# Performance work log

Hardware: AMD Instinct MI355X
Metric: run time of the kernel (lower is better)

The kernel has to match this reference:

```python
import jax, jax.numpy as jnp
import numpy as np


def blockdiag_matmul(x, w):
    """Block-diagonal (Monarch) linear: w has shape (nblocks, out_blk, in_blk);
    x has shape (..., nblocks*in_blk); returns (..., nblocks*out_blk)."""
    nb, q, p = w.shape
    lead = x.shape[:-1]
    xb = x.reshape(-1, nb, p)  # (tokens, nblocks, in_blk)
    out = jnp.einsum('bnp,nqp->bnq', xb, w)  # per-block matmul
    return out.reshape(*lead, nb * q)


def setup_inputs() -> dict:
    key = jax.random.key(0)
    k_x, k1, k2, k3 = jax.random.split(key, 4)
    B, S, D = 4, 4096, 2048
    NB, FF = 4, 8192  # nblocks, adjusted intermediate size
    # Kaiming-uniform-like scale for block weights (fan_in = D or FF per block-row)
    s1 = 1.0 / np.sqrt(D)
    s2 = 1.0 / np.sqrt(FF)
    return {
        'x': jax.random.normal(k_x, (B, S, D), dtype=jnp.float32),
        'w1': jax.random.normal(k1, (NB, FF // NB, D // NB), dtype=jnp.float32) * s1,
        'w3': jax.random.normal(k3, (NB, FF // NB, D // NB), dtype=jnp.float32) * s1,
        'w2': jax.random.normal(k2, (NB, D // NB, FF // NB), dtype=jnp.float32) * s2,
    }


def reference(x, w1, w3, w2):
    # SwiGLU MLP: w2(silu(w1(x)) * w3(x)), all projections block-diagonal
    gate = jax.nn.silu(blockdiag_matmul(x, w1))
    up = blockdiag_matmul(x, w3)
    return blockdiag_matmul(gate * up, w2)
```

## Files before the change

### kernel.cpp

```cpp
#include <hip/hip_runtime.h>
#include <cstdint>

typedef __attribute__((ext_vector_type(8))) short bf16x8;
typedef __attribute__((ext_vector_type(4))) float f32x4;
typedef unsigned short u16;

#define RD(p) (*(const bf16x8*)(p))

__device__ inline u16 f2bf(float f) {
  union { float f; unsigned int u; } v; v.f = f;
  unsigned int u = v.u;
  unsigned int r = (u + 0x7fffu + ((u >> 16) & 1u)) >> 16;
  return (u16)r;
}

__device__ inline void gload_lds16(const u16* g, u16* l) {
  __builtin_amdgcn_global_load_lds(
      (const __attribute__((address_space(1))) void*)g,
      (__attribute__((address_space(3))) void*)l, 16, 0, 0);
}

#define PH_BEGIN() \
  __builtin_amdgcn_s_barrier(); \
  asm volatile("s_waitcnt lgkmcnt(0)" ::: "memory"); \
  __builtin_amdgcn_s_setprio(1)
#define PH_END() \
  __builtin_amdgcn_s_setprio(0); \
  __builtin_amdgcn_s_barrier()

__global__ void cvt_f32_bf16(const float* __restrict__ src, u16* __restrict__ dst, int n8) {
  int i = blockIdx.x * blockDim.x + threadIdx.x;
  int stride = gridDim.x * blockDim.x;
  for (; i < n8; i += stride) {
    const float4* s = (const float4*)(src + (size_t)i * 8);
    float4 a = s[0], b = s[1];
    union { u16 h[8]; uint4 v; } o;
    o.h[0] = f2bf(a.x); o.h[1] = f2bf(a.y); o.h[2] = f2bf(a.z); o.h[3] = f2bf(a.w);
    o.h[4] = f2bf(b.x); o.h[5] = f2bf(b.y); o.h[6] = f2bf(b.z); o.h[7] = f2bf(b.w);
    *(uint4*)(dst + (size_t)i * 8) = o.v;
  }
}

__launch_bounds__(512, 2)
__global__ void gemm_gateup8(const u16* __restrict__ xb, const u16* __restrict__ w1b,
                             const u16* __restrict__ w3b, u16* __restrict__ hout) {
  constexpr int NT = 8;
  __shared__ __attribute__((aligned(16))) u16 lA[2][256 * 64];
  __shared__ __attribute__((aligned(16))) u16 lB[2][2][128 * 64];

  int bid = blockIdx.x;
  int sw = (bid & 7) * 512 + (bid >> 3);
  int nblk = sw >> 10;
  int rem = sw & 1023;
  int mt = rem >> 4, nt = rem & 15;

  int tid = threadIdx.x, w = tid >> 6, ln = tid & 63;
  int wr = w >> 1, wc = w & 1;
  int l15 = ln & 15, l4 = ln >> 4;
  int lr = ln >> 3, ln8 = ln & 7;

  int cx0 = ((l4 ^ (l15 & 7)) << 4);
  int cx1 = (((4 + l4) ^ (l15 & 7)) << 4);
  int aOff0 = (wr * 64 + l15) * 128 + cx0;
  int aOff1 = (wr * 64 + l15) * 128 + cx1;
  int bOff0 = (wc * 64 + l15) * 128 + cx0;
  int bOff1 = (wc * 64 + l15) * 128 + cx1;

  int u0t = w * 8, u1t = 64 + w * 8;
  int rbA0 = ((u0t >> 5) << 6) + (u0t & 31);
  int rbA1 = ((u1t >> 5) << 6) + (u1t & 31);
  int dA0 = rbA0 * 128, dA1 = rbA1 * 128;
  int dB0 = u0t * 128, dB1 = u1t * 128;
  int gaA0 = rbA0 * 2048, gaA1 = rbA1 * 2048;
  int gaB0 = u0t * 512, gaB1 = u1t * 512;
  int swzg = (ln8 ^ lr) << 3;

  const u16* gA  = xb  + (size_t)(mt * 256) * 2048 + nblk * 512 + lr * 2048 + swzg;
  const u16* gB1 = w1b + (size_t)nblk * (2048 * 512) + (size_t)(nt * 128) * 512 + lr * 512 + swzg;
  const u16* gB3 = w3b + (size_t)nblk * (2048 * 512) + (size_t)(nt * 128) * 512 + lr * 512 + swzg;

  f32x4 acc1[4][4], acc3[4][4];
#pragma unroll
  for (int i = 0; i < 4; i++)
#pragma unroll
    for (int j = 0; j < 4; j++) {
      acc1[i][j] = (f32x4){0.f, 0.f, 0.f, 0.f};
      acc3[i][j] = (f32x4){0.f, 0.f, 0.f, 0.f};
    }

  gload_lds16(gA + gaA0,          (u16*)((char*)lA + dA0));
  gload_lds16(gA + gaA1,          (u16*)((char*)lA + dA1));
  gload_lds16(gB3 + gaB0,         (u16*)((char*)lB + 16384 + dB0));
  gload_lds16(gB3 + gaB1,         (u16*)((char*)lB + 16384 + dB1));
  gload_lds16(gA + gaA0 + 65536,  (u16*)((char*)lA + dA0 + 4096));
  gload_lds16(gA + gaA1 + 65536,  (u16*)((char*)lA + dA1 + 4096));
  gload_lds16(gB1 + gaB0,         (u16*)((char*)lB + dB0));
  gload_lds16(gB1 + gaB1,         (u16*)((char*)lB + dB1));
  gload_lds16(gA + 64 + gaA0,         (u16*)((char*)lA + 32768 + dA0));
  gload_lds16(gA + 64 + gaA1,         (u16*)((char*)lA + 32768 + dA1));
  gload_lds16(gB3 + 64 + gaB0,        (u16*)((char*)lB + 32768 + 16384 + dB0));
  gload_lds16(gB3 + 64 + gaB1,        (u16*)((char*)lB + 32768 + 16384 + dB1));
  gload_lds16(gA + 64 + gaA0 + 65536, (u16*)((char*)lA + 32768 + dA0 + 4096));
  gload_lds16(gA + 64 + gaA1 + 65536, (u16*)((char*)lA + 32768 + dA1 + 4096));
  gA += 128; gB3 += 128; gB1 += 64;
  asm volatile("s_waitcnt vmcnt(6)" ::: "memory");
  __builtin_amdgcn_s_barrier();

  int sCur = 0, sNxt = 32768;
  bf16x8 aT[2][2], aH[2][2], b1[4][2], b3[4][2];

  for (int kt = 0; kt < NT; ++kt) {
    const char* pA0 = (const char*)lA + (sCur + aOff0);
    const char* pA1 = (const char*)lA + (sCur + aOff1);
    const char* pB0 = (const char*)lB + (sCur + bOff0);
    const char* pB1p = (const char*)lB + (sCur + bOff1);
    bool s1 = (kt + 1 < NT), s2 = (kt + 2 < NT);

#pragma unroll
    for (int f = 0; f < 2; ++f) {
      aT[f][0] = RD(pA0 + f * 2048); aT[f][1] = RD(pA1 + f * 2048);
    }
#pragma unroll
    for (int g = 0; g < 4; ++g) {
      b1[g][0] = RD(pB0 + g * 2048); b1[g][1] = RD(pB1p + g * 2048);
    }
    if (s1) {
      gload_lds16(gB1 + gaB0, (u16*)((char*)lB + sNxt + dB0));
      gload_lds16(gB1 + gaB1, (u16*)((char*)lB + sNxt + dB1));
    }
    asm volatile("s_waitcnt lgkmcnt(8)" ::: "memory");
    PH_BEGIN();
#pragma unroll
    for (int f = 0; f < 2; ++f)
#pragma unroll
      for (int g = 0; g < 4; ++g)
#pragma unroll
        for (int ks = 0; ks < 2; ++ks)
          acc1[f][g] = __builtin_amdgcn_mfma_f32_16x16x32_bf16(aT[f][ks], b1[g][ks], acc1[f][g], 0, 0, 0);
    PH_END();

#pragma unroll
    for (int g = 0; g < 4; ++g) {
      b3[g][0] = RD(pB0 + 16384 + g * 2048); b3[g][1] = RD(pB1p + 16384 + g * 2048);
    }
    if (s2) {
      gload_lds16(gA + gaA0, (u16*)((char*)lA + sCur + dA0));
      gload_lds16(gA + gaA1, (u16*)((char*)lA + sCur + dA1));
    }
    PH_BEGIN();
#pragma unroll
    for (int f = 0; f < 2; ++f)
#pragma unroll
      for (int g = 0; g < 4; ++g)
#pragma unroll
        for (int ks = 0; ks < 2; ++ks)
          acc3[f][g] = __builtin_amdgcn_mfma_f32_16x16x32_bf16(aT[f][ks], b3[g][ks], acc3[f][g], 0, 0, 0);
    PH_END();

#pragma unroll
    for (int f = 0; f < 2; ++f) {
      aH[f][0] = RD(pA0 + 4096 + f * 2048); aH[f][1] = RD(pA1 + 4096 + f * 2048);
    }
    if (s2) {
      gload_lds16(gB3 + gaB0, (u16*)((char*)lB + sCur + 16384 + dB0));
      gload_lds16(gB3 + gaB1, (u16*)((char*)lB + sCur + 16384 + dB1));
    }
    PH_BEGIN();
#pragma unroll
    for (int f = 0; f < 2; ++f)
#pragma unroll
      for (int g = 0; g < 4; ++g)
#pragma unroll
        for (int ks = 0; ks < 2; ++ks)
          acc1[2 + f][g] = __builtin_amdgcn_mfma_f32_16x16x32_bf16(aH[f][ks], b1[g][ks], acc1[2 + f][g], 0, 0, 0);
    PH_END();

    if (s2) {
      gload_lds16(gA + gaA0 + 65536, (u16*)((char*)lA + sCur + dA0 + 4096));
      gload_lds16(gA + gaA1 + 65536, (u16*)((char*)lA + sCur + dA1 + 4096));
    }
    PH_BEGIN();
#pragma unroll
    for (int f = 0; f < 2; ++f)
#pragma unroll
      for (int g = 0; g < 4; ++g)
#pragma unroll
        for (int ks = 0; ks < 2; ++ks)
          acc3[2 + f][g] = __builtin_amdgcn_mfma_f32_16x16x32_bf16(aH[f][ks], b3[g][ks], acc3[2 + f][g], 0, 0, 0);
    __builtin_amdgcn_s_setprio(0);
    if (kt < NT - 2)       asm volatile("s_waitcnt vmcnt(6)" ::: "memory");
    else if (kt == NT - 2) asm volatile("s_waitcnt vmcnt(0)" ::: "memory");
    __builtin_amdgcn_s_barrier();
    gA += 64; gB1 += 64; gB3 += 64;
    sCur ^= 32768; sNxt ^= 32768;
  }

  u16* Hb = hout + (size_t)(mt * 256 + wr * 64) * 8192 + nblk * 2048 + nt * 128 + wc * 64;
#pragma unroll
  for (int f = 0; f < 4; ++f)
#pragma unroll
    for (int g = 0; g < 4; ++g) {
      int col = g * 16 + l15;
#pragma unroll
      for (int r = 0; r < 4; ++r) {
        int row = f * 16 + l4 * 4 + r;
        float gate = acc1[f][g][r];
        float up = acc3[f][g][r];
        float s = gate * __builtin_amdgcn_rcpf(1.f + __expf(-gate));
        Hb[(size_t)row * 8192 + col] = f2bf(s * up);
      }
    }
}

__launch_bounds__(512, 2)
__global__ void gemm_down8(const u16* __restrict__ hmat, const u16* __restrict__ w2b,
                           float* __restrict__ out) {
  constexpr int NT = 32;
  __shared__ __attribute__((aligned(16))) u16 lA[2][256 * 64];
  __shared__ __attribute__((aligned(16))) u16 lB[2][256 * 64];

  int bid = blockIdx.x;
  int sw = (bid & 7) * 64 + (bid >> 3);
  int nblk = sw >> 7;
  int rem = sw & 127;
  int mt = rem >> 1, nt = rem & 1;

  int tid = threadIdx.x, w = tid >> 6, ln = tid & 63;
  int mi = w >> 2, nj = w & 3;
  int l15 = ln & 15, l4 = ln >> 4;
  int lr = ln >> 3, ln8 = ln & 7;

  int cx0 = ((l4 ^ (l15 & 7)) << 4);
  int cx1 = (((4 + l4) ^ (l15 & 7)) << 4);
  int aOff0 = (mi * 128 + l15) * 128 + cx0;
  int aOff1 = (mi * 128 + l15) * 128 + cx1;
  int bOff0 = (nj * 64 + l15) * 128 + cx0;
  int bOff1 = (nj * 64 + l15) * 128 + cx1;

  int u0t = w * 8, u1t = 64 + w * 8;
  int dA0 = u0t * 128, dA1 = (64 + u1t) * 128;
  int rbB0 = ((u0t >> 5) << 6) + (u0t & 31);
  int rbB1 = ((u1t >> 5) << 6) + (u1t & 31);
  int dB0 = rbB0 * 128, dB1 = rbB1 * 128;
  int gaA0 = u0t * 8192, gaA1 = (64 + u1t) * 8192;
  int gaB0 = rbB0 * 2048, gaB1 = rbB1 * 2048;
  int swzg = (ln8 ^ lr) << 3;

  const u16* gA = hmat + (size_t)(mt * 256) * 8192 + nblk * 2048 + lr * 8192 + swzg;
  const u16* gB = w2b + (size_t)nblk * (512 * 2048) + (size_t)(nt * 256) * 2048 + lr * 2048 + swzg;

  f32x4 acc[8][4];
#pragma unroll
  for (int i = 0; i < 8; i++)
#pragma unroll
    for (int j = 0; j < 4; j++) acc[i][j] = (f32x4){0.f, 0.f, 0.f, 0.f};

  gload_lds16(gA + gaA0,           (u16*)((char*)lA + dA0));
  gload_lds16(gA + gaA1,           (u16*)((char*)lA + dA1));
  gload_lds16(gB + gaB0 + 65536,   (u16*)((char*)lB + dB0 + 4096));
  gload_lds16(gB + gaB1 + 65536,   (u16*)((char*)lB + dB1 + 4096));
  gload_lds16(gA + gaA0 + 524288,  (u16*)((char*)lA + dA0 + 8192));
  gload_lds16(gA + gaA1 + 524288,  (u16*)((char*)lA + dA1 + 8192));
  gload_lds16(gB + gaB0,           (u16*)((char*)lB + dB0));
  gload_lds16(gB + gaB1,           (u16*)((char*)lB + dB1));
  gload_lds16(gA + 64 + gaA0,          (u16*)((char*)lA + 32768 + dA0));
  gload_lds16(gA + 64 + gaA1,          (u16*)((char*)lA + 32768 + dA1));
  gload_lds16(gB + 64 + gaB0 + 65536,  (u16*)((char*)lB + 32768 + dB0 + 4096));
  gload_lds16(gB + 64 + gaB1 + 65536,  (u16*)((char*)lB + 32768 + dB1 + 4096));
  gload_lds16(gA + 64 + gaA0 + 524288, (u16*)((char*)lA + 32768 + dA0 + 8192));
  gload_lds16(gA + 64 + gaA1 + 524288, (u16*)((char*)lA + 32768 + dA1 + 8192));
  gA += 128; gB += 64;
  asm volatile("s_waitcnt vmcnt(6)" ::: "memory");
  __builtin_amdgcn_s_barrier();

  int sCur = 0, sNxt = 32768;
  bf16x8 aF[4][2], bLo[2][2], bHi[2][2];

  for (int kt = 0; kt < NT; ++kt) {
    const char* pA0 = (const char*)lA + (sCur + aOff0);
    const char* pA1 = (const char*)lA + (sCur + aOff1);
    const char* pB0 = (const char*)lB + (sCur + bOff0);
    const char* pB1p = (const char*)lB + (sCur + bOff1);
    bool s1 = (kt + 1 < NT), s2 = (kt + 2 < NT);

#pragma unroll
    for (int f = 0; f < 4; ++f) {
      aF[f][0] = RD(pA0 + f * 2048); aF[f][1] = RD(pA1 + f * 2048);
    }
#pragma unroll
    for (int g = 0; g < 2; ++g) {
      bLo[g][0] = RD(pB0 + g * 2048); bLo[g][1] = RD(pB1p + g * 2048);
    }
    if (s1) {
      gload_lds16(gB + gaB0, (u16*)((char*)lB + sNxt + dB0));
      gload_lds16(gB + gaB1, (u16*)((char*)lB + sNxt + dB1));
    }
    asm volatile("s_waitcnt lgkmcnt(8)" ::: "memory");
    PH_BEGIN();
#pragma unroll
    for (int f = 0; f < 4; ++f)
#pragma unroll
      for (int g = 0; g < 2; ++g)
#pragma unroll
        for (int ks = 0; ks < 2; ++ks)
          acc[f][g] = __builtin_amdgcn_mfma_f32_16x16x32_bf16(aF[f][ks], bLo[g][ks], acc[f][g], 0, 0, 0);
    PH_END();

#pragma unroll
    for (int g = 0; g < 2; ++g) {
      bHi[g][0] = RD(pB0 + 4096 + g * 2048); bHi[g][1] = RD(pB1p + 4096 + g * 2048);
    }
    if (s2) {
      gload_lds16(gA + gaA0, (u16*)((char*)lA + sCur + dA0));
      gload_lds16(gA + gaA1, (u16*)((char*)lA + sCur + dA1));
    }
    PH_BEGIN();
#pragma unroll
    for (int f = 0; f < 4; ++f)
#pragma unroll
      for (int g = 0; g < 2; ++g)
#pragma unroll
        for (int ks = 0; ks < 2; ++ks)
          acc[f][2 + g] = __builtin_amdgcn_mfma_f32_16x16x32_bf16(aF[f][ks], bHi[g][ks], acc[f][2 + g], 0, 0, 0);
    PH_END();

#pragma unroll
    for (int f = 0; f < 4; ++f) {
      aF[f][0] = RD(pA0 + 8192 + f * 2048); aF[f][1] = RD(pA1 + 8192 + f * 2048);
    }
    if (s2) {
      gload_lds16(gB + 64 + gaB0 + 65536, (u16*)((char*)lB + sCur + dB0 + 4096));
      gload_lds16(gB + 64 + gaB1 + 65536, (u16*)((char*)lB + sCur + dB1 + 4096));
    }
    PH_BEGIN();
#pragma unroll
    for (int f = 0; f < 4; ++f)
#pragma unroll
      for (int g = 0; g < 2; ++g)
#pragma unroll
        for (int ks = 0; ks < 2; ++ks)
          acc[4 + f][g] = __builtin_amdgcn_mfma_f32_16x16x32_bf16(aF[f][ks], bLo[g][ks], acc[4 + f][g], 0, 0, 0);
    PH_END();

    if (s2) {
      gload_lds16(gA + gaA0 + 524288, (u16*)((char*)lA + sCur + dA0 + 8192));
      gload_lds16(gA + gaA1 + 524288, (u16*)((char*)lA + sCur + dA1 + 8192));
    }
    PH_BEGIN();
#pragma unroll
    for (int f = 0; f < 4; ++f)
#pragma unroll
      for (int g = 0; g < 2; ++g)
#pragma unroll
        for (int ks = 0; ks < 2; ++ks)
          acc[4 + f][2 + g] = __builtin_amdgcn_mfma_f32_16x16x32_bf16(aF[f][ks], bHi[g][ks], acc[4 + f][2 + g], 0, 0, 0);
    __builtin_amdgcn_s_setprio(0);
    if (kt < NT - 2)       asm volatile("s_waitcnt vmcnt(6)" ::: "memory");
    else if (kt == NT - 2) asm volatile("s_waitcnt vmcnt(0)" ::: "memory");
    __builtin_amdgcn_s_barrier();
    gA += 64; gB += 64;
    sCur ^= 32768; sNxt ^= 32768;
  }

  float* Ob = out + (size_t)(mt * 256 + mi * 128) * 2048 + nblk * 512 + nt * 256 + nj * 64;
#pragma unroll
  for (int f = 0; f < 8; ++f)
#pragma unroll
    for (int g = 0; g < 4; ++g) {
      int col = g * 16 + l15;
#pragma unroll
      for (int r = 0; r < 4; ++r) {
        int row = f * 16 + l4 * 4 + r;
        Ob[(size_t)row * 2048 + col] = acc[f][g][r];
      }
    }
}

extern "C" void kernel_launch(void* const* d_in, const int* in_sizes, int n_in,
                              void* d_out, int out_size, void* d_ws, size_t ws_size,
                              hipStream_t stream) {
  const float* x  = (const float*)d_in[0];
  const float* w1 = (const float*)d_in[1];
  const float* w3 = (const float*)d_in[2];
  const float* w2 = (const float*)d_in[3];

  char* ws = (char*)d_ws;
  u16* xb  = (u16*)(ws);
  u16* w1b = (u16*)(ws + 67108864);
  u16* w3b = (u16*)(ws + 75497472);
  u16* w2b = (u16*)(ws + 83886080);
  u16* h   = (u16*)(ws + 92274688);

  cvt_f32_bf16<<<2048, 256, 0, stream>>>(x,  xb,  33554432 / 8);
  cvt_f32_bf16<<<2048, 256, 0, stream>>>(w1, w1b, 4194304 / 8);
  cvt_f32_bf16<<<2048, 256, 0, stream>>>(w3, w3b, 4194304 / 8);
  cvt_f32_bf16<<<2048, 256, 0, stream>>>(w2, w2b, 4194304 / 8);

  gemm_gateup8<<<4096, 512, 0, stream>>>(xb, w1b, w3b, h);
  gemm_down8<<<512, 512, 0, stream>>>(h, w2b, (float*)d_out);
}
```

Measured before the change: 556.7 us.

## Process multiple output tiles per block with continuous cross-tile prefetch pipeline

Both GEMM kernels now loop over several output tiles per workgroup (4 N-tiles in gate/up, 2 M-tiles in down). The grid shrinks accordingly, and the global-to-LDS prefetch pipeline runs across tile boundaries, so the next tile's loads overlap the current tile's tail and epilogue. This removes the per-block prologue and pipeline-drain cost and cuts launch tail effects. In exchange, epilogue stores now sit inside the main loop, and the down kernel has only 256 blocks, which may underfill the GPU.

```diff
diff --git a/kernel.cpp b/kernel.cpp
--- a/kernel.cpp
+++ b/kernel.cpp
@@ -45,14 +45,16 @@
 __global__ void gemm_gateup8(const u16* __restrict__ xb, const u16* __restrict__ w1b,
                              const u16* __restrict__ w3b, u16* __restrict__ hout) {
   constexpr int NT = 8;
+  constexpr int TPB = 4;
+  constexpr int TOT = NT * TPB;
   __shared__ __attribute__((aligned(16))) u16 lA[2][256 * 64];
   __shared__ __attribute__((aligned(16))) u16 lB[2][2][128 * 64];
 
   int bid = blockIdx.x;
-  int sw = (bid & 7) * 512 + (bid >> 3);
-  int nblk = sw >> 10;
-  int rem = sw & 1023;
-  int mt = rem >> 4, nt = rem & 15;
+  int sw = (bid & 7) * 128 + (bid >> 3);
+  int nblk = sw >> 8;
+  int rem = sw & 255;
+  int mt = rem >> 2, ntg = rem & 3;
 
   int tid = threadIdx.x, w = tid >> 6, ln = tid & 63;
   int wr = w >> 1, wc = w & 1;
@@ -76,8 +78,11 @@
   int swzg = (ln8 ^ lr) << 3;
 
   const u16* gA  = xb  + (size_t)(mt * 256) * 2048 + nblk * 512 + lr * 2048 + swzg;
-  const u16* gB1 = w1b + (size_t)nblk * (2048 * 512) + (size_t)(nt * 128) * 512 + lr * 512 + swzg;
-  const u16* gB3 = w3b + (size_t)nblk * (2048 * 512) + (size_t)(nt * 128) * 512 + lr * 512 + swzg;
+  const u16* gB1 = w1b + (size_t)nblk * (2048 * 512) + (size_t)(ntg * 512) * 512 + lr * 512 + swzg;
+  const u16* gB3 = w3b + (size_t)nblk * (2048 * 512) + (size_t)(ntg * 512) * 512 + lr * 512 + swzg;
+
+  #define OFFA(s) (((s) & 7) * 64)
+  #define OFFB(s) ((((s) >> 3) << 16) + (((s) & 7) * 64))
 
   f32x4 acc1[4][4], acc3[4][4];
 #pragma unroll
@@ -88,33 +93,34 @@
       acc3[i][j] = (f32x4){0.f, 0.f, 0.f, 0.f};
     }
 
-  gload_lds16(gA + gaA0,          (u16*)((char*)lA + dA0));
-  gload_lds16(gA + gaA1,          (u16*)((char*)lA + dA1));
-  gload_lds16(gB3 + gaB0,         (u16*)((char*)lB + 16384 + dB0));
-  gload_lds16(gB3 + gaB1,         (u16*)((char*)lB + 16384 + dB1));
-  gload_lds16(gA + gaA0 + 65536,  (u16*)((char*)lA + dA0 + 4096));
-  gload_lds16(gA + gaA1 + 65536,  (u16*)((char*)lA + dA1 + 4096));
-  gload_lds16(gB1 + gaB0,         (u16*)((char*)lB + dB0));
-  gload_lds16(gB1 + gaB1,         (u16*)((char*)lB + dB1));
-  gload_lds16(gA + 64 + gaA0,         (u16*)((char*)lA + 32768 + dA0));
-  gload_lds16(gA + 64 + gaA1,         (u16*)((char*)lA + 32768 + dA1));
-  gload_lds16(gB3 + 64 + gaB0,        (u16*)((char*)lB + 32768 + 16384 + dB0));
-  gload_lds16(gB3 + 64 + gaB1,        (u16*)((char*)lB + 32768 + 16384 + dB1));
-  gload_lds16(gA + 64 + gaA0 + 65536, (u16*)((char*)lA + 32768 + dA0 + 4096));
-  gload_lds16(gA + 64 + gaA1 + 65536, (u16*)((char*)lA + 32768 + dA1 + 4096));
-  gA += 128; gB3 += 128; gB1 += 64;
+  gload_lds16(gA + gaA0,              (u16*)((char*)lA + dA0));
+  gload_lds16(gA + gaA1,              (u16*)((char*)lA + dA1));
+  gload_lds16(gB3 + gaB0,             (u16*)((char*)lB + 16384 + dB0));
+  gload_lds16(gB3 + gaB1,             (u16*)((char*)lB + 16384 + dB1));
+  gload_lds16(gA + gaA0 + 65536,      (u16*)((char*)lA + dA0 + 4096));
+  gload_lds16(gA + gaA1 + 65536,      (u16*)((char*)lA + dA1 + 4096));
+  gload_lds16(gB1 + gaB0,             (u16*)((char*)lB + dB0));
+  gload_lds16(gB1 + gaB1,             (u16*)((char*)lB + dB1));
+  gload_lds16(gA + OFFA(1) + gaA0,          (u16*)((char*)lA + 32768 + dA0));
+  gload_lds16(gA + OFFA(1) + gaA1,          (u16*)((char*)lA + 32768 + dA1));
+  gload_lds16(gB3 + OFFB(1) + gaB0,         (u16*)((char*)lB + 32768 + 16384 + dB0));
+  gload_lds16(gB3 + OFFB(1) + gaB1,         (u16*)((char*)lB + 32768 + 16384 + dB1));
+  gload_lds16(gA + OFFA(1) + gaA0 + 65536,  (u16*)((char*)lA + 32768 + dA0 + 4096));
+  gload_lds16(gA + OFFA(1) + gaA1 + 65536,  (u16*)((char*)lA + 32768 + dA1 + 4096));
   asm volatile("s_waitcnt vmcnt(6)" ::: "memory");
   __builtin_amdgcn_s_barrier();
 
   int sCur = 0, sNxt = 32768;
   bf16x8 aT[2][2], aH[2][2], b1[4][2], b3[4][2];
 
-  for (int kt = 0; kt < NT; ++kt) {
+  for (int kt = 0; kt < TOT; ++kt) {
     const char* pA0 = (const char*)lA + (sCur + aOff0);
     const char* pA1 = (const char*)lA + (sCur + aOff1);
     const char* pB0 = (const char*)lB + (sCur + bOff0);
     const char* pB1p = (const char*)lB + (sCur + bOff1);
-    bool s1 = (kt + 1 < NT), s2 = (kt + 2 < NT);
+    int s1 = kt + 1, s2 = kt + 2;
+    int oA2 = OFFA(s2), oB1n = OFFB(s1), oB32 = OFFB(s2);
+    bool q1 = (s1 < TOT), q2 = (s2 < TOT);
 
 #pragma unroll
     for (int f = 0; f < 2; ++f) {
@@ -124,9 +130,9 @@
     for (int g = 0; g < 4; ++g) {
       b1[g][0] = RD(pB0 + g * 2048); b1[g][1] = RD(pB1p + g * 2048);
     }
-    if (s1) {
-      gload_lds16(gB1 + gaB0, (u16*)((char*)lB + sNxt + dB0));
-      gload_lds16(gB1 + gaB1, (u16*)((char*)lB + sNxt + dB1));
+    if (q1) {
+      gload_lds16(gB1 + oB1n + gaB0, (u16*)((char*)lB + sNxt + dB0));
+      gload_lds16(gB1 + oB1n + gaB1, (u16*)((char*)lB + sNxt + dB1));
     }
     asm volatile("s_waitcnt lgkmcnt(8)" ::: "memory");
     PH_BEGIN();
@@ -143,9 +149,9 @@
     for (int g = 0; g < 4; ++g) {
       b3[g][0] = RD(pB0 + 16384 + g * 2048); b3[g][1] = RD(pB1p + 16384 + g * 2048);
     }
-    if (s2) {
-      gload_lds16(gA + gaA0, (u16*)((char*)lA + sCur + dA0));
-      gload_lds16(gA + gaA1, (u16*)((char*)lA + sCur + dA1));
+    if (q2) {
+      gload_lds16(gA + oA2 + gaA0, (u16*)((char*)lA + sCur + dA0));
+      gload_lds16(gA + oA2 + gaA1, (u16*)((char*)lA + sCur + dA1));
     }
     PH_BEGIN();
 #pragma unroll
@@ -161,9 +167,9 @@
     for (int f = 0; f < 2; ++f) {
       aH[f][0] = RD(pA0 + 4096 + f * 2048); aH[f][1] = RD(pA1 + 4096 + f * 2048);
     }
-    if (s2) {
-      gload_lds16(gB3 + gaB0, (u16*)((char*)lB + sCur + 16384 + dB0));
-      gload_lds16(gB3 + gaB1, (u16*)((char*)lB + sCur + 16384 + dB1));
+    if (q2) {
+      gload_lds16(gB3 + oB32 + gaB0, (u16*)((char*)lB + sCur + 16384 + dB0));
+      gload_lds16(gB3 + oB32 + gaB1, (u16*)((char*)lB + sCur + 16384 + dB1));
     }
     PH_BEGIN();
 #pragma unroll
@@ -175,9 +181,9 @@
           acc1[2 + f][g] = __builtin_amdgcn_mfma_f32_16x16x32_bf16(aH[f][ks], b1[g][ks], acc1[2 + f][g], 0, 0, 0);
     PH_END();
 
-    if (s2) {
-      gload_lds16(gA + gaA0 + 65536, (u16*)((char*)lA + sCur + dA0 + 4096));
-      gload_lds16(gA + gaA1 + 65536, (u16*)((char*)lA + sCur + dA1 + 4096));
+    if (q2) {
+      gload_lds16(gA + oA2 + gaA0 + 65536, (u16*)((char*)lA + sCur + dA0 + 4096));
+      gload_lds16(gA + oA2 + gaA1 + 65536, (u16*)((char*)lA + sCur + dA1 + 4096));
     }
     PH_BEGIN();
 #pragma unroll
@@ -188,42 +194,55 @@
         for (int ks = 0; ks < 2; ++ks)
           acc3[2 + f][g] = __builtin_amdgcn_mfma_f32_16x16x32_bf16(aH[f][ks], b3[g][ks], acc3[2 + f][g], 0, 0, 0);
     __builtin_amdgcn_s_setprio(0);
-    if (kt < NT - 2)       asm volatile("s_waitcnt vmcnt(6)" ::: "memory");
-    else if (kt == NT - 2) asm volatile("s_waitcnt vmcnt(0)" ::: "memory");
+    if (kt < TOT - 2)       asm volatile("s_waitcnt vmcnt(6)" ::: "memory");
+    else if (kt == TOT - 2) asm volatile("s_waitcnt vmcnt(0)" ::: "memory");
     __builtin_amdgcn_s_barrier();
-    gA += 64; gB1 += 64; gB3 += 64;
     sCur ^= 32768; sNxt ^= 32768;
+
+    if ((kt & 7) == 7) {
+      int nt = ntg * 4 + (kt >> 3);
+      u16* Hb = hout + (size_t)(mt * 256 + wr * 64) * 8192 + nblk * 2048 + nt * 128 + wc * 64;
+#pragma unroll
+      for (int f = 0; f < 4; ++f)
+#pragma unroll
+        for (int g = 0; g < 4; ++g) {
+          int col = g * 16 + l15;
+#pragma unroll
+          for (int r = 0; r < 4; ++r) {
+            int row = f * 16 + l4 * 4 + r;
+            float gate = acc1[f][g][r];
+            float up = acc3[f][g][r];
+            float s = gate * __builtin_amdgcn_rcpf(1.f + __expf(-gate));
+            Hb[(size_t)row * 8192 + col] = f2bf(s * up);
+          }
+        }
+#pragma unroll
+      for (int i = 0; i < 4; i++)
+#pragma unroll
+        for (int j = 0; j < 4; j++) {
+          acc1[i][j] = (f32x4){0.f, 0.f, 0.f, 0.f};
+          acc3[i][j] = (f32x4){0.f, 0.f, 0.f, 0.f};
+        }
+    }
   }
-
-  u16* Hb = hout + (size_t)(mt * 256 + wr * 64) * 8192 + nblk * 2048 + nt * 128 + wc * 64;
-#pragma unroll
-  for (int f = 0; f < 4; ++f)
-#pragma unroll
-    for (int g = 0; g < 4; ++g) {
-      int col = g * 16 + l15;
-#pragma unroll
-      for (int r = 0; r < 4; ++r) {
-        int row = f * 16 + l4 * 4 + r;
-        float gate = acc1[f][g][r];
-        float up = acc3[f][g][r];
-        float s = gate * __builtin_amdgcn_rcpf(1.f + __expf(-gate));
-        Hb[(size_t)row * 8192 + col] = f2bf(s * up);
-      }
-    }
+  #undef OFFA
+  #undef OFFB
 }
 
 __launch_bounds__(512, 2)
 __global__ void gemm_down8(const u16* __restrict__ hmat, const u16* __restrict__ w2b,
                            float* __restrict__ out) {
   constexpr int NT = 32;
+  constexpr int TPB = 2;
+  constexpr int TOT = NT * TPB;
   __shared__ __attribute__((aligned(16))) u16 lA[2][256 * 64];
   __shared__ __attribute__((aligned(16))) u16 lB[2][256 * 64];
 
   int bid = blockIdx.x;
-  int sw = (bid & 7) * 64 + (bid >> 3);
-  int nblk = sw >> 7;
-  int rem = sw & 127;
-  int mt = rem >> 1, nt = rem & 1;
+  int sw = (bid & 7) * 32 + (bid >> 3);
+  int nblk = sw >> 6;
+  int rem = sw & 63;
+  int mtg = rem >> 1, nt = rem & 1;
 
   int tid = threadIdx.x, w = tid >> 6, ln = tid & 63;
   int mi = w >> 2, nj = w & 3;
@@ -246,42 +265,46 @@
   int gaB0 = rbB0 * 2048, gaB1 = rbB1 * 2048;
   int swzg = (ln8 ^ lr) << 3;
 
-  const u16* gA = hmat + (size_t)(mt * 256) * 8192 + nblk * 2048 + lr * 8192 + swzg;
+  const u16* gA = hmat + (size_t)(mtg * 512) * 8192 + nblk * 2048 + lr * 8192 + swzg;
   const u16* gB = w2b + (size_t)nblk * (512 * 2048) + (size_t)(nt * 256) * 2048 + lr * 2048 + swzg;
 
+  #define OFFA(s) ((((s) >> 5) << 21) + (((s) & 31) * 64))
+  #define OFFB(s) (((s) & 31) * 64)
+
   f32x4 acc[8][4];
 #pragma unroll
   for (int i = 0; i < 8; i++)
 #pragma unroll
     for (int j = 0; j < 4; j++) acc[i][j] = (f32x4){0.f, 0.f, 0.f, 0.f};
 
-  gload_lds16(gA + gaA0,           (u16*)((char*)lA + dA0));
-  gload_lds16(gA + gaA1,           (u16*)((char*)lA + dA1));
-  gload_lds16(gB + gaB0 + 65536,   (u16*)((char*)lB + dB0 + 4096));
-  gload_lds16(gB + gaB1 + 65536,   (u16*)((char*)lB + dB1 + 4096));
-  gload_lds16(gA + gaA0 + 524288,  (u16*)((char*)lA + dA0 + 8192));
-  gload_lds16(gA + gaA1 + 524288,  (u16*)((char*)lA + dA1 + 8192));
-  gload_lds16(gB + gaB0,           (u16*)((char*)lB + dB0));
-  gload_lds16(gB + gaB1,           (u16*)((char*)lB + dB1));
-  gload_lds16(gA + 64 + gaA0,          (u16*)((char*)lA + 32768 + dA0));
-  gload_lds16(gA + 64 + gaA1,          (u16*)((char*)lA + 32768 + dA1));
-  gload_lds16(gB + 64 + gaB0 + 65536,  (u16*)((char*)lB + 32768 + dB0 + 4096));
-  gload_lds16(gB + 64 + gaB1 + 65536,  (u16*)((char*)lB + 32768 + dB1 + 4096));
-  gload_lds16(gA + 64 + gaA0 + 524288, (u16*)((char*)lA + 32768 + dA0 + 8192));
-  gload_lds16(gA + 64 + gaA1 + 524288, (u16*)((char*)lA + 32768 + dA1 + 8192));
-  gA += 128; gB += 64;
+  gload_lds16(gA + gaA0,             (u16*)((char*)lA + dA0));
+  gload_lds16(gA + gaA1,             (u16*)((char*)lA + dA1));
+  gload_lds16(gB + gaB0 + 65536,     (u16*)((char*)lB + dB0 + 4096));
+  gload_lds16(gB + gaB1 + 65536,     (u16*)((char*)lB + dB1 + 4096));
+  gload_lds16(gA + gaA0 + 524288,    (u16*)((char*)lA + dA0 + 8192));
+  gload_lds16(gA + gaA1 + 524288,    (u16*)((char*)lA + dA1 + 8192));
+  gload_lds16(gB + gaB0,             (u16*)((char*)lB + dB0));
+  gload_lds16(gB + gaB1,             (u16*)((char*)lB + dB1));
+  gload_lds16(gA + OFFA(1) + gaA0,            (u16*)((char*)lA + 32768 + dA0));
+  gload_lds16(gA + OFFA(1) + gaA1,            (u16*)((char*)lA + 32768 + dA1));
+  gload_lds16(gB + OFFB(1) + gaB0 + 65536,    (u16*)((char*)lB + 32768 + dB0 + 4096));
+  gload_lds16(gB + OFFB(1) + gaB1 + 65536,    (u16*)((char*)lB + 32768 + dB1 + 4096));
+  gload_lds16(gA + OFFA(1) + gaA0 + 524288,   (u16*)((char*)lA + 32768 + dA0 + 8192));
+  gload_lds16(gA + OFFA(1) + gaA1 + 524288,   (u16*)((char*)lA + 32768 + dA1 + 8192));
   asm volatile("s_waitcnt vmcnt(6)" ::: "memory");
   __builtin_amdgcn_s_barrier();
 
   int sCur = 0, sNxt = 32768;
   bf16x8 aF[4][2], bLo[2][2], bHi[2][2];
 
-  for (int kt = 0; kt < NT; ++kt) {
+  for (int kt = 0; kt < TOT; ++kt) {
     const char* pA0 = (const char*)lA + (sCur + aOff0);
     const char* pA1 = (const char*)lA + (sCur + aOff1);
     const char* pB0 = (const char*)lB + (sCur + bOff0);
     const char* pB1p = (const char*)lB + (sCur + bOff1);
-    bool s1 = (kt + 1 < NT), s2 = (kt + 2 < NT);
+    int s1 = kt + 1, s2 = kt + 2;
+    int oA2 = OFFA(s2), oBn = OFFB(s1), oB2 = OFFB(s2);
+    bool q1 = (s1 < TOT), q2 = (s2 < TOT);
 
 #pragma unroll
     for (int f = 0; f < 4; ++f) {
@@ -291,9 +314,9 @@
     for (int g = 0; g < 2; ++g) {
       bLo[g][0] = RD(pB0 + g * 2048); bLo[g][1] = RD(pB1p + g * 2048);
     }
-    if (s1) {
-      gload_lds16(gB + gaB0, (u16*)((char*)lB + sNxt + dB0));
-      gload_lds16(gB + gaB1, (u16*)((char*)lB + sNxt + dB1));
+    if (q1) {
+      gload_lds16(gB + oBn + gaB0, (u16*)((char*)lB + sNxt + dB0));
+      gload_lds16(gB + oBn + gaB1, (u16*)((char*)lB + sNxt + dB1));
     }
     asm volatile("s_waitcnt lgkmcnt(8)" ::: "memory");
     PH_BEGIN();
@@ -310,9 +333,9 @@
     for (int g = 0; g < 2; ++g) {
       bHi[g][0] = RD(pB0 + 4096 + g * 2048); bHi[g][1] = RD(pB1p + 4096 + g * 2048);
     }
-    if (s2) {
-      gload_lds16(gA + gaA0, (u16*)((char*)lA + sCur + dA0));
-      gload_lds16(gA + gaA1, (u16*)((char*)lA + sCur + dA1));
+    if (q2) {
+      gload_lds16(gA + oA2 + gaA0, (u16*)((char*)lA + sCur + dA0));
+      gload_lds16(gA + oA2 + gaA1, (u16*)((char*)lA + sCur + dA1));
     }
     PH_BEGIN();
 #pragma unroll
@@ -328,9 +351,9 @@
     for (int f = 0; f < 4; ++f) {
       aF[f][0] = RD(pA0 + 8192 + f * 2048); aF[f][1] = RD(pA1 + 8192 + f * 2048);
     }
-    if (s2) {
-      gload_lds16(gB + 64 + gaB0 + 65536, (u16*)((char*)lB + sCur + dB0 + 4096));
-      gload_lds16(gB + 64 + gaB1 + 65536, (u16*)((char*)lB + sCur + dB1 + 4096));
+    if (q2) {
+      gload_lds16(gB + oB2 + gaB0 + 65536, (u16*)((char*)lB + sCur + dB0 + 4096));
+      gload_lds16(gB + oB2 + gaB1 + 65536, (u16*)((char*)lB + sCur + dB1 + 4096));
     }
     PH_BEGIN();
 #pragma unroll
@@ -342,9 +365,9 @@
           acc[4 + f][g] = __builtin_amdgcn_mfma_f32_16x16x32_bf16(aF[f][ks], bLo[g][ks], acc[4 + f][g], 0, 0, 0);
     PH_END();
 
-    if (s2) {
-      gload_lds16(gA + gaA0 + 524288, (u16*)((char*)lA + sCur + dA0 + 8192));
-      gload_lds16(gA + gaA1 + 524288, (u16*)((char*)lA + sCur + dA1 + 8192));
+    if (q2) {
+      gload_lds16(gA + oA2 + gaA0 + 524288, (u16*)((char*)lA + sCur + dA0 + 8192));
+      gload_lds16(gA + oA2 + gaA1 + 524288, (u16*)((char*)lA + sCur + dA1 + 8192));
     }
     PH_BEGIN();
 #pragma unroll
@@ -355,25 +378,33 @@
         for (int ks = 0; ks < 2; ++ks)
           acc[4 + f][2 + g] = __builtin_amdgcn_mfma_f32_16x16x32_bf16(aF[f][ks], bHi[g][ks], acc[4 + f][2 + g], 0, 0, 0);
     __builtin_amdgcn_s_setprio(0);
-    if (kt < NT - 2)       asm volatile("s_waitcnt vmcnt(6)" ::: "memory");
-    else if (kt == NT - 2) asm volatile("s_waitcnt vmcnt(0)" ::: "memory");
+    if (kt < TOT - 2)       asm volatile("s_waitcnt vmcnt(6)" ::: "memory");
+    else if (kt == TOT - 2) asm volatile("s_waitcnt vmcnt(0)" ::: "memory");
     __builtin_amdgcn_s_barrier();
-    gA += 64; gB += 64;
     sCur ^= 32768; sNxt ^= 32768;
+
+    if ((kt & 31) == 31) {
+      int mtt = mtg * 2 + (kt >> 5);
+      float* Ob = out + (size_t)(mtt * 256 + mi * 128) * 2048 + nblk * 512 + nt * 256 + nj * 64;
+#pragma unroll
+      for (int f = 0; f < 8; ++f)
+#pragma unroll
+        for (int g = 0; g < 4; ++g) {
+          int col = g * 16 + l15;
+#pragma unroll
+          for (int r = 0; r < 4; ++r) {
+            int row = f * 16 + l4 * 4 + r;
+            Ob[(size_t)row * 2048 + col] = acc[f][g][r];
+          }
+        }
+#pragma unroll
+      for (int i = 0; i < 8; i++)
+#pragma unroll
+        for (int j = 0; j < 4; j++) acc[i][j] = (f32x4){0.f, 0.f, 0.f, 0.f};
+    }
   }
-
-  float* Ob = out + (size_t)(mt * 256 + mi * 128) * 2048 + nblk * 512 + nt * 256 + nj * 64;
-#pragma unroll
-  for (int f = 0; f < 8; ++f)
-#pragma unroll
-    for (int g = 0; g < 4; ++g) {
-      int col = g * 16 + l15;
-#pragma unroll
-      for (int r = 0; r < 4; ++r) {
-        int row = f * 16 + l4 * 4 + r;
-        Ob[(size_t)row * 2048 + col] = acc[f][g][r];
-      }
-    }
+  #undef OFFA
+  #undef OFFB
 }
 
 extern "C" void kernel_launch(void* const* d_in, const int* in_sizes, int n_in,
@@ -396,6 +427,6 @@
   cvt_f32_bf16<<<2048, 256, 0, stream>>>(w3, w3b, 4194304 / 8);
   cvt_f32_bf16<<<2048, 256, 0, stream>>>(w2, w2b, 4194304 / 8);
 
-  gemm_gateup8<<<4096, 512, 0, stream>>>(xb, w1b, w3b, h);
-  gemm_down8<<<512, 512, 0, stream>>>(h, w2b, (float*)d_out);
-}
+  gemm_gateup8<<<1024, 512, 0, stream>>>(xb, w1b, w3b, h);
+  gemm_down8<<<256, 512, 0, stream>>>(h, w2b, (float*)d_out);
+}
```

New measurement: 950.6 us. 1.71x slower.
